# Kernel tuning notes

Hardware: AMD Instinct MI355X
Metric: run time of the kernel (lower is better)

## Reference

```python
import jax, jax.numpy as jnp
import numpy as np

B, CIN, T, H, W = 2, 256, 16, 16, 8
FF, COUT, NHEADS = 512, 256, 8
TEMP = 16.0
BN_EPS = 1e-5


def setup_inputs() -> dict:
    key = jax.random.key(0)
    ks = jax.random.split(key, 6)
    s_in = 1.0 / np.sqrt(CIN)
    s_ff = 1.0 / np.sqrt(FF)
    return {
        "x": jax.random.normal(ks[0], (B, CIN, T, H, W), jnp.float32),
        "WK": jax.random.uniform(ks[1], (FF, CIN), jnp.float32, -s_in, s_in),
        "WQ": jax.random.uniform(ks[2], (FF, CIN), jnp.float32, -s_in, s_in),
        "WV": jax.random.uniform(ks[3], (FF, CIN), jnp.float32, -s_in, s_in),
        "Wo": jax.random.uniform(ks[4], (COUT, FF), jnp.float32, -s_ff, s_ff),
        "bo": jax.random.uniform(ks[5], (COUT,), jnp.float32, -s_ff, s_ff),
        "gamma": jnp.ones((COUT,), jnp.float32),
        "beta": jnp.zeros((COUT,), jnp.float32),
    }


def reference(x, WK, WQ, WV, Wo, bo, gamma, beta):
    N = T * H * W
    xf = x.reshape(B, CIN, N)  # 1x1 conv3d == channel matmul
    dh = FF // NHEADS
    K = jnp.einsum("fc,bcn->bfn", WK, xf).reshape(B, NHEADS, dh, N)
    Q = jnp.einsum("fc,bcn->bfn", WQ, xf).reshape(B, NHEADS, dh, N)
    V = jnp.einsum("fc,bcn->bfn", WV, xf).reshape(B, NHEADS, dh, N)
    # KQ[b,h,i,j] = K_i . Q_j  (i = key token, j = query token, as in torch)
    KQ = jnp.einsum("bhdi,bhdj->bhij", K, Q) / TEMP
    # block-causal mask: token time index t = token_idx // (H*W); tril -> allow i >= j
    t_idx = jnp.arange(N) // (H * W)
    allow = t_idx[:, None] >= t_idx[None, :]  # (N, N)
    KQ = jnp.where(allow[None, None], KQ, -jnp.inf)
    attn = jax.nn.softmax(KQ, axis=3)  # softmax over j (last dim), as in torch
    # out[b,h,d,i] = sum_j V[b,h,d,j] * attn[b,h,i,j]
    Vo = jnp.einsum("bhdj,bhij->bhdi", V, attn).reshape(B, FF, N)
    y = jnp.einsum("of,bfn->bon", Wo, Vo) + bo[None, :, None]
    y = jax.nn.relu(y).reshape(B, COUT, T, H, W)
    out = x + y  # skip: out_dim == in_dim
    # BatchNorm3d (training-mode batch stats, biased var)
    mean = out.mean(axis=(0, 2, 3, 4), keepdims=True)
    var = out.var(axis=(0, 2, 3, 4), keepdims=True)
    norm = (out - mean) * jax.lax.rsqrt(var + BN_EPS)
    return norm * gamma[None, :, None, None, None] + beta[None, :, None, None, None]
```

## Files before the change

kernel.cpp:

```cpp
#include <hip/hip_runtime.h>
#include <math.h>

#define BB_   2
#define CIN_  256
#define NTOK_ 2048
#define FF_   512
#define COUT_ 256
#define NH_   8
#define DH_   64
#define HW_   128
#define BNEPS_ 1e-5f
#define SCALE_LOG2_ 0.09016844005556021f

typedef __attribute__((ext_vector_type(8))) short short8;
typedef __attribute__((ext_vector_type(4))) float f32x4;

__device__ inline unsigned short f2bf(float f) {
  union { float f; unsigned u; } v; v.f = f;
  unsigned r = (v.u + 0x7FFF + ((v.u >> 16) & 1)) >> 16;
  return (unsigned short)r;
}

__device__ __forceinline__ void dma16(const unsigned short* g, unsigned short* l) {
  __builtin_amdgcn_global_load_lds(
      (const __attribute__((address_space(1))) void*)g,
      (__attribute__((address_space(3))) void*)l, 16, 0, 0);
}

__global__ __launch_bounds__(256) void prep_kernel(
    const float* __restrict__ x, const float* __restrict__ WK,
    const float* __restrict__ WQ, const float* __restrict__ WV,
    const float* __restrict__ Wo, unsigned short* __restrict__ xT,
    unsigned short* __restrict__ Wkb, unsigned short* __restrict__ Wqb,
    unsigned short* __restrict__ Wvb, unsigned short* __restrict__ Wob) {
  __shared__ float T[64 * 65];
  const int tid = threadIdx.x;
  const int bid = blockIdx.x;
  if (bid < 256) {
    const int b = bid >> 7;
    const int rem = bid & 127;
    const int n0 = (rem >> 2) * 64;
    const int c0 = (rem & 3) * 64;
#pragma unroll
    for (int p = 0; p < 4; ++p) {
      const int idx = tid + 256 * p;
      const int row = idx >> 4, col = (idx & 15) * 4;
      const float4 v =
          *(const float4*)(x + (size_t)(b * CIN_ + c0 + row) * NTOK_ + n0 + col);
      T[row * 65 + col + 0] = v.x; T[row * 65 + col + 1] = v.y;
      T[row * 65 + col + 2] = v.z; T[row * 65 + col + 3] = v.w;
    }
    __syncthreads();
#pragma unroll
    for (int p = 0; p < 2; ++p) {
      const int idx = tid + 256 * p;
      const int nl = idx >> 3, c8 = (idx & 7) * 8;
      unsigned short u[8];
#pragma unroll
      for (int i = 0; i < 8; ++i) u[i] = f2bf(T[(c8 + i) * 65 + nl]);
      *(uint4*)(xT + ((size_t)(b * NTOK_ + n0 + nl)) * CIN_ + c0 + c8) =
          *(uint4*)u;
    }
  } else {
    const int t = bid - 256;
    const int which = t >> 5, blk = t & 31;
    const float* src = which == 0 ? WK : which == 1 ? WQ : which == 2 ? WV : Wo;
    unsigned short* dst = which == 0 ? Wkb : which == 1 ? Wqb : which == 2 ? Wvb : Wob;
    const int base = blk * 4096 + tid * 16;
#pragma unroll
    for (int p = 0; p < 4; ++p) {
      const float4 v = *(const float4*)(src + base + p * 4);
      ushort4 u;
      u.x = f2bf(v.x); u.y = f2bf(v.y); u.z = f2bf(v.z); u.w = f2bf(v.w);
      *(ushort4*)(dst + base + p * 4) = u;
    }
  }
}

__global__ __launch_bounds__(256, 2) void qkv_kernel(
    const unsigned short* __restrict__ xT, const unsigned short* __restrict__ Wkb,
    const unsigned short* __restrict__ Wqb, const unsigned short* __restrict__ Wvb,
    unsigned short* __restrict__ Kb, unsigned short* __restrict__ Qb,
    unsigned short* __restrict__ Vt) {
  __shared__ unsigned short Wsh[128 * 72];
  __shared__ unsigned short Xsh[128 * 72];
  const int tid = threadIdx.x;
  const int lane = tid & 63, w = tid >> 6;
  const int lx = lane & 15, q = lane >> 4;
  const int wm = w >> 1, wn = w & 1;
  const int n0 = blockIdx.x * 128;
  const int f0 = blockIdx.y * 128;
  const int b = blockIdx.z / 3, which = blockIdx.z % 3;
  const unsigned short* Wb = which == 0 ? Wkb : which == 1 ? Wqb : Wvb;

  const int srow = tid >> 3;
  const int soff = (tid & 7) * 8;
  const unsigned short* Wg = Wb + (size_t)(f0 + srow) * CIN_ + soff;
  const unsigned short* Xg = xT + ((size_t)(b * NTOK_ + n0 + srow)) * CIN_ + soff;

  uint4 wr[4], xr[4];
#pragma unroll
  for (int r = 0; r < 4; ++r) {
    wr[r] = *(const uint4*)(Wg + (size_t)(32 * r) * CIN_);
    xr[r] = *(const uint4*)(Xg + (size_t)(32 * r) * CIN_);
  }

  f32x4 acc[4][4];
#pragma unroll
  for (int i = 0; i < 4; ++i)
#pragma unroll
    for (int j = 0; j < 4; ++j) acc[i][j] = (f32x4){0.f, 0.f, 0.f, 0.f};

  for (int kk = 0; kk < 4; ++kk) {
    __syncthreads();
#pragma unroll
    for (int r = 0; r < 4; ++r) {
      *(uint4*)(Wsh + (srow + 32 * r) * 72 + soff) = wr[r];
      *(uint4*)(Xsh + (srow + 32 * r) * 72 + soff) = xr[r];
    }
    if (kk < 3) {
      const int c0 = (kk + 1) * 64;
#pragma unroll
      for (int r = 0; r < 4; ++r) {
        wr[r] = *(const uint4*)(Wg + (size_t)(32 * r) * CIN_ + c0);
        xr[r] = *(const uint4*)(Xg + (size_t)(32 * r) * CIN_ + c0);
      }
    }
    __syncthreads();
    short8 xF[4][2];
#pragma unroll
    for (int i = 0; i < 4; ++i) {
      xF[i][0] = *(const short8*)(Xsh + (64 * wn + 16 * i + lx) * 72 + q * 8);
      xF[i][1] = *(const short8*)(Xsh + (64 * wn + 16 * i + lx) * 72 + 32 + q * 8);
    }
    if (which < 2) {
#pragma unroll
      for (int i = 0; i < 4; ++i) {
        const short8 w0 = *(const short8*)(Wsh + (64 * wm + 16 * i + lx) * 72 + q * 8);
        const short8 w1 = *(const short8*)(Wsh + (64 * wm + 16 * i + lx) * 72 + 32 + q * 8);
#pragma unroll
        for (int j = 0; j < 4; ++j) {
          acc[i][j] = __builtin_amdgcn_mfma_f32_16x16x32_bf16(w0, xF[j][0], acc[i][j], 0, 0, 0);
          acc[i][j] = __builtin_amdgcn_mfma_f32_16x16x32_bf16(w1, xF[j][1], acc[i][j], 0, 0, 0);
        }
      }
    } else {
#pragma unroll
      for (int j = 0; j < 4; ++j) {
        const short8 w0 = *(const short8*)(Wsh + (64 * wm + 16 * j + lx) * 72 + q * 8);
        const short8 w1 = *(const short8*)(Wsh + (64 * wm + 16 * j + lx) * 72 + 32 + q * 8);
#pragma unroll
        for (int i = 0; i < 4; ++i) {
          acc[i][j] = __builtin_amdgcn_mfma_f32_16x16x32_bf16(xF[i][0], w0, acc[i][j], 0, 0, 0);
          acc[i][j] = __builtin_amdgcn_mfma_f32_16x16x32_bf16(xF[i][1], w1, acc[i][j], 0, 0, 0);
        }
      }
    }
  }

  const int h = (f0 >> 6) + wm;
  if (which < 2) {
    unsigned short* Y = (which == 0 ? Kb : Qb);
    const float sc = (which == 0) ? SCALE_LOG2_ : 1.0f;
#pragma unroll
    for (int i = 0; i < 4; ++i)
#pragma unroll
      for (int j = 0; j < 4; ++j) {
        const int n = n0 + 64 * wn + 16 * j + lx;
        const int d0 = 16 * i + 4 * q;
        ushort4 u;
        u.x = f2bf(acc[i][j][0] * sc); u.y = f2bf(acc[i][j][1] * sc);
        u.z = f2bf(acc[i][j][2] * sc); u.w = f2bf(acc[i][j][3] * sc);
        *(ushort4*)(Y + ((size_t)((b * NH_ + h) * NTOK_ + n)) * DH_ + d0) = u;
      }
  } else {
#pragma unroll
    for (int i = 0; i < 4; ++i)
#pragma unroll
      for (int j = 0; j < 4; ++j) {
        const int d = 16 * j + lx;
        const int n = n0 + 64 * wn + 16 * i + 4 * q;
        ushort4 u;
        u.x = f2bf(acc[i][j][0]); u.y = f2bf(acc[i][j][1]);
        u.z = f2bf(acc[i][j][2]); u.w = f2bf(acc[i][j][3]);
        *(ushort4*)(Vt + ((size_t)((b * NH_ + h) * DH_ + d)) * NTOK_ + n) = u;
      }
  }
}

__global__ __launch_bounds__(256, 3) void attn_kernel(
    const unsigned short* __restrict__ Kb, const unsigned short* __restrict__ Qb,
    const unsigned short* __restrict__ Vt, unsigned short* __restrict__ Ob) {
  __shared__ __align__(16) unsigned short Qbuf[2][4096];
  __shared__ __align__(16) unsigned short Vbuf[2][4096];
  __shared__ __align__(16) unsigned short Psh[4 * 16 * 72];

  const int tid = threadIdx.x;
  const int lane = tid & 63;
  const int w = tid >> 6;
  const int lx = lane & 15;
  const int q = lane >> 4;

  const int bid = blockIdx.x;
  const int u = bid >> 4;
  const int iblk = (u < 16) ? (31 - u) : (u - 16);
  const int bh = bid & 15;
  const int h = bh & 7, b = bh >> 3;
  const int i0 = iblk * 64;
  const int njt = ((iblk >> 1) + 1) * 2;

  const size_t bhs = (size_t)b * NH_ + h;
  const unsigned short* Kg = Kb + bhs * (size_t)NTOK_ * DH_ + (size_t)i0 * DH_;
  const unsigned short* Qg = Qb + bhs * (size_t)NTOK_ * DH_;
  const unsigned short* Vg = Vt + bhs * (size_t)DH_ * NTOK_;

  const int drow_lo = (lane >> 3);
  const int dcg = (lane & 7) ^ drow_lo;

  auto stage = [&](int buf, int j0) {
#pragma unroll
    for (int cc = 0; cc < 2; ++cc) {
      const int chunk = 2 * w + cc;
      const int row = chunk * 8 + drow_lo;
      dma16(Qg + (size_t)(j0 + row) * DH_ + dcg * 8, &Qbuf[buf][chunk * 512]);
      dma16(Vg + (size_t)row * NTOK_ + j0 + dcg * 8, &Vbuf[buf][chunk * 512]);
    }
  };

  const short8 aK0 = *(const short8*)(Kg + (16 * w + lx) * DH_ + q * 8);
  const short8 aK1 = *(const short8*)(Kg + (16 * w + lx) * DH_ + 32 + q * 8);

  unsigned short* Pw = Psh + w * 16 * 72;

  f32x4 o[4];
#pragma unroll
  for (int s = 0; s < 4; ++s) o[s] = (f32x4){0.f, 0.f, 0.f, 0.f};
  float rsum[4] = {0.f, 0.f, 0.f, 0.f};

  const int fr0 = ((q ^ (lx & 7)) << 3);
  const int fr1 = (((4 + q) ^ (lx & 7)) << 3);

  stage(0, 0);
  __syncthreads();

  int cur = 0;
  for (int jt = 0; jt < njt; ++jt) {
    if (jt + 1 < njt) stage(cur ^ 1, (jt + 1) * 64);

    const unsigned short* Qs = Qbuf[cur];
    const unsigned short* Vs = Vbuf[cur];

    f32x4 sa[4];
#pragma unroll
    for (int s = 0; s < 4; ++s) {
      const int row = 16 * s + lx;
      const short8 b0 = *(const short8*)(Qs + row * 64 + fr0);
      const short8 b1 = *(const short8*)(Qs + row * 64 + fr1);
      sa[s] = (f32x4){0.f, 0.f, 0.f, 0.f};
      sa[s] = __builtin_amdgcn_mfma_f32_16x16x32_bf16(aK0, b0, sa[s], 0, 0, 0);
      sa[s] = __builtin_amdgcn_mfma_f32_16x16x32_bf16(aK1, b1, sa[s], 0, 0, 0);
    }

#pragma unroll
    for (int s = 0; s < 4; ++s)
#pragma unroll
      for (int r = 0; r < 4; ++r) {
        const float p = __builtin_amdgcn_exp2f(sa[s][r]);
        rsum[r] += p;
        Pw[(q * 4 + r) * 72 + 16 * s + lx] =
            (unsigned short)(__builtin_bit_cast(unsigned, p) >> 16);
      }
    asm volatile("s_waitcnt lgkmcnt(0)" ::: "memory");

    const short8 pb0 = *(const short8*)(Pw + lx * 72 + q * 8);
    const short8 pb1 = *(const short8*)(Pw + lx * 72 + 32 + q * 8);
#pragma unroll
    for (int s = 0; s < 4; ++s) {
      const int row = 16 * s + lx;
      const short8 va0 = *(const short8*)(Vs + row * 64 + fr0);
      const short8 va1 = *(const short8*)(Vs + row * 64 + fr1);
      o[s] = __builtin_amdgcn_mfma_f32_16x16x32_bf16(va0, pb0, o[s], 0, 0, 0);
      o[s] = __builtin_amdgcn_mfma_f32_16x16x32_bf16(va1, pb1, o[s], 0, 0, 0);
    }

    __syncthreads();
    cur ^= 1;
  }

#pragma unroll
  for (int r = 0; r < 4; ++r) {
#pragma unroll
    for (int off = 1; off < 16; off <<= 1) rsum[r] += __shfl_xor(rsum[r], off);
  }
  const int gsrc = ((lx >> 2) << 4);
  const float u0 = __shfl(rsum[0], gsrc);
  const float u1 = __shfl(rsum[1], gsrc);
  const float u2 = __shfl(rsum[2], gsrc);
  const float u3 = __shfl(rsum[3], gsrc);
  const float lsel = (lx & 2) ? ((lx & 1) ? u3 : u2) : ((lx & 1) ? u1 : u0);
  const float invl = 1.0f / lsel;
  const int n = i0 + 16 * w + lx;
#pragma unroll
  for (int s = 0; s < 4; ++s) {
    ushort4 uo;
    uo.x = f2bf(o[s][0] * invl); uo.y = f2bf(o[s][1] * invl);
    uo.z = f2bf(o[s][2] * invl); uo.w = f2bf(o[s][3] * invl);
    *(ushort4*)(Ob + ((size_t)(b * NTOK_ + n)) * FF_ + h * 64 + 16 * s + 4 * q) = uo;
  }
}

__global__ __launch_bounds__(256) void proj_kernel(
    const unsigned short* __restrict__ Ob, const unsigned short* __restrict__ Wob,
    const float* __restrict__ bo, const float* __restrict__ x,
    float* __restrict__ pre) {
  __shared__ unsigned short Osh[64 * 72];
  __shared__ unsigned short Wsh[64 * 72];
  const int tid = threadIdx.x;
  const int lane = tid & 63, w = tid >> 6;
  const int lx = lane & 15, q = lane >> 4;
  const int wn = w & 1, wo = w >> 1;
  const int n0 = blockIdx.x * 64;
  const int o0 = blockIdx.y * 64;
  const int b = blockIdx.z;

  const int srow = tid >> 3;
  const int soff = (tid & 7) * 8;
  const unsigned short* Og = Ob + ((size_t)(b * NTOK_ + n0 + srow)) * FF_ + soff;
  const unsigned short* Wg = Wob + (size_t)(o0 + srow) * FF_ + soff;

  uint4 orr[2], wrr[2];
#pragma unroll
  for (int r = 0; r < 2; ++r) {
    orr[r] = *(const uint4*)(Og + (size_t)(32 * r) * FF_);
    wrr[r] = *(const uint4*)(Wg + (size_t)(32 * r) * FF_);
  }

  f32x4 acc[2][2];
#pragma unroll
  for (int i = 0; i < 2; ++i)
#pragma unroll
    for (int j = 0; j < 2; ++j) acc[i][j] = (f32x4){0.f, 0.f, 0.f, 0.f};

  for (int kk = 0; kk < 8; ++kk) {
    __syncthreads();
#pragma unroll
    for (int r = 0; r < 2; ++r) {
      *(uint4*)(Osh + (srow + 32 * r) * 72 + soff) = orr[r];
      *(uint4*)(Wsh + (srow + 32 * r) * 72 + soff) = wrr[r];
    }
    if (kk < 7) {
      const int c0 = (kk + 1) * 64;
#pragma unroll
      for (int r = 0; r < 2; ++r) {
        orr[r] = *(const uint4*)(Og + (size_t)(32 * r) * FF_ + c0);
        wrr[r] = *(const uint4*)(Wg + (size_t)(32 * r) * FF_ + c0);
      }
    }
    __syncthreads();
    short8 aF[2][2], bF[2][2];
#pragma unroll
    for (int i = 0; i < 2; ++i) {
      aF[i][0] = *(const short8*)(Osh + (32 * wn + 16 * i + lx) * 72 + q * 8);
      aF[i][1] = *(const short8*)(Osh + (32 * wn + 16 * i + lx) * 72 + 32 + q * 8);
      bF[i][0] = *(const short8*)(Wsh + (32 * wo + 16 * i + lx) * 72 + q * 8);
      bF[i][1] = *(const short8*)(Wsh + (32 * wo + 16 * i + lx) * 72 + 32 + q * 8);
    }
#pragma unroll
    for (int i = 0; i < 2; ++i)
#pragma unroll
      for (int j = 0; j < 2; ++j) {
        acc[i][j] = __builtin_amdgcn_mfma_f32_16x16x32_bf16(aF[i][0], bF[j][0], acc[i][j], 0, 0, 0);
        acc[i][j] = __builtin_amdgcn_mfma_f32_16x16x32_bf16(aF[i][1], bF[j][1], acc[i][j], 0, 0, 0);
      }
  }

#pragma unroll
  for (int j = 0; j < 2; ++j) {
    const int o = o0 + 32 * wo + 16 * j + lx;
    const float bias = bo[o];
#pragma unroll
    for (int i = 0; i < 2; ++i) {
      const int n = n0 + 32 * wn + 16 * i + 4 * q;
      const float4 xv = *(const float4*)(x + ((size_t)(b * CIN_ + o)) * NTOK_ + n);
      float4 v;
      v.x = fmaxf(acc[i][j][0] + bias, 0.f) + xv.x;
      v.y = fmaxf(acc[i][j][1] + bias, 0.f) + xv.y;
      v.z = fmaxf(acc[i][j][2] + bias, 0.f) + xv.z;
      v.w = fmaxf(acc[i][j][3] + bias, 0.f) + xv.w;
      *(float4*)(pre + ((size_t)(b * COUT_ + o)) * NTOK_ + n) = v;
    }
  }
}

__global__ __launch_bounds__(256) void bn_kernel(
    float* __restrict__ out, const float* __restrict__ gamma,
    const float* __restrict__ beta) {
  __shared__ float red[8];
  const int c = blockIdx.x;
  const int tid = threadIdx.x;
  const int lane = tid & 63, w = tid >> 6;

  float4 v[2][2];
  float s = 0.f, s2 = 0.f;
#pragma unroll
  for (int b = 0; b < BB_; ++b) {
    float* base = out + ((size_t)(b * COUT_ + c)) * NTOK_;
#pragma unroll
    for (int p = 0; p < 2; ++p) {
      const float4 t = *(const float4*)(base + 4 * tid + p * 1024);
      v[b][p] = t;
      s += t.x + t.y + t.z + t.w;
      s2 += t.x * t.x + t.y * t.y + t.z * t.z + t.w * t.w;
    }
  }
#pragma unroll
  for (int off = 32; off >= 1; off >>= 1) {
    s += __shfl_xor(s, off);
    s2 += __shfl_xor(s2, off);
  }
  if (lane == 0) { red[w] = s; red[4 + w] = s2; }
  __syncthreads();
  const float S = red[0] + red[1] + red[2] + red[3];
  const float S2 = red[4] + red[5] + red[6] + red[7];
  const float inv = 1.0f / (float)(BB_ * NTOK_);
  const float mean = S * inv;
  const float var = S2 * inv - mean * mean;
  const float sc = rsqrtf(var + BNEPS_) * gamma[c];
  const float bt = beta[c];
#pragma unroll
  for (int b = 0; b < BB_; ++b) {
    float* base = out + ((size_t)(b * COUT_ + c)) * NTOK_;
#pragma unroll
    for (int p = 0; p < 2; ++p) {
      float4 t = v[b][p];
      t.x = (t.x - mean) * sc + bt;
      t.y = (t.y - mean) * sc + bt;
      t.z = (t.z - mean) * sc + bt;
      t.w = (t.w - mean) * sc + bt;
      *(float4*)(base + 4 * tid + p * 1024) = t;
    }
  }
}

extern "C" void kernel_launch(void* const* d_in, const int* in_sizes, int n_in,
                              void* d_out, int out_size, void* d_ws, size_t ws_size,
                              hipStream_t stream) {
  (void)in_sizes; (void)n_in; (void)out_size; (void)ws_size;
  const float* x = (const float*)d_in[0];
  const float* WK = (const float*)d_in[1];
  const float* WQ = (const float*)d_in[2];
  const float* WV = (const float*)d_in[3];
  const float* Wo = (const float*)d_in[4];
  const float* bo = (const float*)d_in[5];
  const float* gamma = (const float*)d_in[6];
  const float* beta = (const float*)d_in[7];

  char* ws = (char*)d_ws;
  unsigned short* xT  = (unsigned short*)(ws);
  unsigned short* Wkb = (unsigned short*)(ws + 2097152);
  unsigned short* Wqb = (unsigned short*)(ws + 2359296);
  unsigned short* Wvb = (unsigned short*)(ws + 2621440);
  unsigned short* Wob = (unsigned short*)(ws + 2883584);
  unsigned short* Kb  = (unsigned short*)(ws + 3145728);
  unsigned short* Qb  = (unsigned short*)(ws + 7340032);
  unsigned short* Vt  = (unsigned short*)(ws + 11534336);
  unsigned short* Ob  = (unsigned short*)(ws + 15728640);
  float* out = (float*)d_out;

  prep_kernel<<<384, 256, 0, stream>>>(x, WK, WQ, WV, Wo, xT, Wkb, Wqb, Wvb, Wob);
  qkv_kernel<<<dim3(16, 4, 6), 256, 0, stream>>>(xT, Wkb, Wqb, Wvb, Kb, Qb, Vt);
  attn_kernel<<<dim3(512, 1, 1), 256, 0, stream>>>(Kb, Qb, Vt, Ob);
  proj_kernel<<<dim3(32, 4, 2), 256, 0, stream>>>(Ob, Wob, bo, x, out);
  bn_kernel<<<256, 256, 0, stream>>>(out, gamma, beta);
}
```

Measured before the change: 146.1 us.

## Halve QKV token tile for more blocks; widen attention key tiles to 128

The QKV projection kernel now uses 64-token tiles instead of 128, which doubles the grid to 768 blocks, and raises its occupancy target to 3. The attention kernel now stages 128-column Q/V tiles per iteration with a re-derived XOR swizzle, which halves the number of loop iterations and barriers, and processes the P·V step in two halves that reuse the per-wave P buffer. The larger attention LDS footprint lowers its occupancy target from 3 to 2 blocks per CU, and the bigger tiles add more work per step on the causal diagonal.

```diff
diff --git a/kernel.cpp b/kernel.cpp
--- a/kernel.cpp
+++ b/kernel.cpp
@@ -77,18 +77,18 @@
   }
 }
 
-__global__ __launch_bounds__(256, 2) void qkv_kernel(
+__global__ __launch_bounds__(256, 3) void qkv_kernel(
     const unsigned short* __restrict__ xT, const unsigned short* __restrict__ Wkb,
     const unsigned short* __restrict__ Wqb, const unsigned short* __restrict__ Wvb,
     unsigned short* __restrict__ Kb, unsigned short* __restrict__ Qb,
     unsigned short* __restrict__ Vt) {
   __shared__ unsigned short Wsh[128 * 72];
-  __shared__ unsigned short Xsh[128 * 72];
+  __shared__ unsigned short Xsh[64 * 72];
   const int tid = threadIdx.x;
   const int lane = tid & 63, w = tid >> 6;
   const int lx = lane & 15, q = lane >> 4;
   const int wm = w >> 1, wn = w & 1;
-  const int n0 = blockIdx.x * 128;
+  const int n0 = blockIdx.x * 64;
   const int f0 = blockIdx.y * 128;
   const int b = blockIdx.z / 3, which = blockIdx.z % 3;
   const unsigned short* Wb = which == 0 ? Wkb : which == 1 ? Wqb : Wvb;
@@ -98,40 +98,37 @@
   const unsigned short* Wg = Wb + (size_t)(f0 + srow) * CIN_ + soff;
   const unsigned short* Xg = xT + ((size_t)(b * NTOK_ + n0 + srow)) * CIN_ + soff;
 
-  uint4 wr[4], xr[4];
-#pragma unroll
-  for (int r = 0; r < 4; ++r) {
-    wr[r] = *(const uint4*)(Wg + (size_t)(32 * r) * CIN_);
-    xr[r] = *(const uint4*)(Xg + (size_t)(32 * r) * CIN_);
-  }
-
-  f32x4 acc[4][4];
+  uint4 wr[4], xr[2];
+#pragma unroll
+  for (int r = 0; r < 4; ++r) wr[r] = *(const uint4*)(Wg + (size_t)(32 * r) * CIN_);
+#pragma unroll
+  for (int r = 0; r < 2; ++r) xr[r] = *(const uint4*)(Xg + (size_t)(32 * r) * CIN_);
+
+  f32x4 acc[4][2];
 #pragma unroll
   for (int i = 0; i < 4; ++i)
 #pragma unroll
-    for (int j = 0; j < 4; ++j) acc[i][j] = (f32x4){0.f, 0.f, 0.f, 0.f};
+    for (int j = 0; j < 2; ++j) acc[i][j] = (f32x4){0.f, 0.f, 0.f, 0.f};
 
   for (int kk = 0; kk < 4; ++kk) {
     __syncthreads();
 #pragma unroll
-    for (int r = 0; r < 4; ++r) {
-      *(uint4*)(Wsh + (srow + 32 * r) * 72 + soff) = wr[r];
-      *(uint4*)(Xsh + (srow + 32 * r) * 72 + soff) = xr[r];
-    }
+    for (int r = 0; r < 4; ++r) *(uint4*)(Wsh + (srow + 32 * r) * 72 + soff) = wr[r];
+#pragma unroll
+    for (int r = 0; r < 2; ++r) *(uint4*)(Xsh + (srow + 32 * r) * 72 + soff) = xr[r];
     if (kk < 3) {
       const int c0 = (kk + 1) * 64;
 #pragma unroll
-      for (int r = 0; r < 4; ++r) {
-        wr[r] = *(const uint4*)(Wg + (size_t)(32 * r) * CIN_ + c0);
-        xr[r] = *(const uint4*)(Xg + (size_t)(32 * r) * CIN_ + c0);
-      }
-    }
-    __syncthreads();
-    short8 xF[4][2];
-#pragma unroll
-    for (int i = 0; i < 4; ++i) {
-      xF[i][0] = *(const short8*)(Xsh + (64 * wn + 16 * i + lx) * 72 + q * 8);
-      xF[i][1] = *(const short8*)(Xsh + (64 * wn + 16 * i + lx) * 72 + 32 + q * 8);
+      for (int r = 0; r < 4; ++r) wr[r] = *(const uint4*)(Wg + (size_t)(32 * r) * CIN_ + c0);
+#pragma unroll
+      for (int r = 0; r < 2; ++r) xr[r] = *(const uint4*)(Xg + (size_t)(32 * r) * CIN_ + c0);
+    }
+    __syncthreads();
+    short8 xF[2][2];
+#pragma unroll
+    for (int i = 0; i < 2; ++i) {
+      xF[i][0] = *(const short8*)(Xsh + (32 * wn + 16 * i + lx) * 72 + q * 8);
+      xF[i][1] = *(const short8*)(Xsh + (32 * wn + 16 * i + lx) * 72 + 32 + q * 8);
     }
     if (which < 2) {
 #pragma unroll
@@ -139,20 +136,20 @@
         const short8 w0 = *(const short8*)(Wsh + (64 * wm + 16 * i + lx) * 72 + q * 8);
         const short8 w1 = *(const short8*)(Wsh + (64 * wm + 16 * i + lx) * 72 + 32 + q * 8);
 #pragma unroll
-        for (int j = 0; j < 4; ++j) {
+        for (int j = 0; j < 2; ++j) {
           acc[i][j] = __builtin_amdgcn_mfma_f32_16x16x32_bf16(w0, xF[j][0], acc[i][j], 0, 0, 0);
           acc[i][j] = __builtin_amdgcn_mfma_f32_16x16x32_bf16(w1, xF[j][1], acc[i][j], 0, 0, 0);
         }
       }
     } else {
 #pragma unroll
-      for (int j = 0; j < 4; ++j) {
-        const short8 w0 = *(const short8*)(Wsh + (64 * wm + 16 * j + lx) * 72 + q * 8);
-        const short8 w1 = *(const short8*)(Wsh + (64 * wm + 16 * j + lx) * 72 + 32 + q * 8);
-#pragma unroll
-        for (int i = 0; i < 4; ++i) {
-          acc[i][j] = __builtin_amdgcn_mfma_f32_16x16x32_bf16(xF[i][0], w0, acc[i][j], 0, 0, 0);
-          acc[i][j] = __builtin_amdgcn_mfma_f32_16x16x32_bf16(xF[i][1], w1, acc[i][j], 0, 0, 0);
+      for (int jf = 0; jf < 4; ++jf) {
+        const short8 w0 = *(const short8*)(Wsh + (64 * wm + 16 * jf + lx) * 72 + q * 8);
+        const short8 w1 = *(const short8*)(Wsh + (64 * wm + 16 * jf + lx) * 72 + 32 + q * 8);
+#pragma unroll
+        for (int i = 0; i < 2; ++i) {
+          acc[jf][i] = __builtin_amdgcn_mfma_f32_16x16x32_bf16(xF[i][0], w0, acc[jf][i], 0, 0, 0);
+          acc[jf][i] = __builtin_amdgcn_mfma_f32_16x16x32_bf16(xF[i][1], w1, acc[jf][i], 0, 0, 0);
         }
       }
     }
@@ -165,8 +162,8 @@
 #pragma unroll
     for (int i = 0; i < 4; ++i)
 #pragma unroll
-      for (int j = 0; j < 4; ++j) {
-        const int n = n0 + 64 * wn + 16 * j + lx;
+      for (int j = 0; j < 2; ++j) {
+        const int n = n0 + 32 * wn + 16 * j + lx;
         const int d0 = 16 * i + 4 * q;
         ushort4 u;
         u.x = f2bf(acc[i][j][0] * sc); u.y = f2bf(acc[i][j][1] * sc);
@@ -175,24 +172,24 @@
       }
   } else {
 #pragma unroll
-    for (int i = 0; i < 4; ++i)
-#pragma unroll
-      for (int j = 0; j < 4; ++j) {
-        const int d = 16 * j + lx;
-        const int n = n0 + 64 * wn + 16 * i + 4 * q;
+    for (int jf = 0; jf < 4; ++jf)
+#pragma unroll
+      for (int i = 0; i < 2; ++i) {
+        const int d = 16 * jf + lx;
+        const int n = n0 + 32 * wn + 16 * i + 4 * q;
         ushort4 u;
-        u.x = f2bf(acc[i][j][0]); u.y = f2bf(acc[i][j][1]);
-        u.z = f2bf(acc[i][j][2]); u.w = f2bf(acc[i][j][3]);
+        u.x = f2bf(acc[jf][i][0]); u.y = f2bf(acc[jf][i][1]);
+        u.z = f2bf(acc[jf][i][2]); u.w = f2bf(acc[jf][i][3]);
         *(ushort4*)(Vt + ((size_t)((b * NH_ + h) * DH_ + d)) * NTOK_ + n) = u;
       }
   }
 }
 
-__global__ __launch_bounds__(256, 3) void attn_kernel(
+__global__ __launch_bounds__(256, 2) void attn_kernel(
     const unsigned short* __restrict__ Kb, const unsigned short* __restrict__ Qb,
     const unsigned short* __restrict__ Vt, unsigned short* __restrict__ Ob) {
-  __shared__ __align__(16) unsigned short Qbuf[2][4096];
-  __shared__ __align__(16) unsigned short Vbuf[2][4096];
+  __shared__ __align__(16) unsigned short Qbuf[2][8192];
+  __shared__ __align__(16) unsigned short Vbuf[2][8192];
   __shared__ __align__(16) unsigned short Psh[4 * 16 * 72];
 
   const int tid = threadIdx.x;
@@ -207,23 +204,27 @@
   const int bh = bid & 15;
   const int h = bh & 7, b = bh >> 3;
   const int i0 = iblk * 64;
-  const int njt = ((iblk >> 1) + 1) * 2;
+  const int njt = (iblk >> 1) + 1;
 
   const size_t bhs = (size_t)b * NH_ + h;
   const unsigned short* Kg = Kb + bhs * (size_t)NTOK_ * DH_ + (size_t)i0 * DH_;
   const unsigned short* Qg = Qb + bhs * (size_t)NTOK_ * DH_;
   const unsigned short* Vg = Vt + bhs * (size_t)DH_ * NTOK_;
 
-  const int drow_lo = (lane >> 3);
-  const int dcg = (lane & 7) ^ drow_lo;
-
   auto stage = [&](int buf, int j0) {
 #pragma unroll
-    for (int cc = 0; cc < 2; ++cc) {
-      const int chunk = 2 * w + cc;
-      const int row = chunk * 8 + drow_lo;
-      dma16(Qg + (size_t)(j0 + row) * DH_ + dcg * 8, &Qbuf[buf][chunk * 512]);
-      dma16(Vg + (size_t)row * NTOK_ + j0 + dcg * 8, &Vbuf[buf][chunk * 512]);
+    for (int cc = 0; cc < 4; ++cc) {
+      const int chunk = 4 * w + cc;
+      {
+        const int row = chunk * 8 + (lane >> 3);
+        const int grp = (lane & 7) ^ (row & 7);
+        dma16(Qg + (size_t)(j0 + row) * DH_ + grp * 8, &Qbuf[buf][chunk * 512]);
+      }
+      {
+        const int row = chunk * 4 + (lane >> 4);
+        const int grp = (lane & 15) ^ (row & 7);
+        dma16(Vg + (size_t)row * NTOK_ + j0 + grp * 8, &Vbuf[buf][chunk * 512]);
+      }
     }
   };
 
@@ -239,20 +240,23 @@
 
   const int fr0 = ((q ^ (lx & 7)) << 3);
   const int fr1 = (((4 + q) ^ (lx & 7)) << 3);
+  int frv[4];
+#pragma unroll
+  for (int kk = 0; kk < 4; ++kk) frv[kk] = (((4 * kk + q) ^ (lx & 7)) << 3);
 
   stage(0, 0);
   __syncthreads();
 
   int cur = 0;
   for (int jt = 0; jt < njt; ++jt) {
-    if (jt + 1 < njt) stage(cur ^ 1, (jt + 1) * 64);
+    if (jt + 1 < njt) stage(cur ^ 1, (jt + 1) * 128);
 
     const unsigned short* Qs = Qbuf[cur];
     const unsigned short* Vs = Vbuf[cur];
 
-    f32x4 sa[4];
-#pragma unroll
-    for (int s = 0; s < 4; ++s) {
+    f32x4 sa[8];
+#pragma unroll
+    for (int s = 0; s < 8; ++s) {
       const int row = 16 * s + lx;
       const short8 b0 = *(const short8*)(Qs + row * 64 + fr0);
       const short8 b1 = *(const short8*)(Qs + row * 64 + fr1);
@@ -262,25 +266,29 @@
     }
 
 #pragma unroll
-    for (int s = 0; s < 4; ++s)
-#pragma unroll
-      for (int r = 0; r < 4; ++r) {
-        const float p = __builtin_amdgcn_exp2f(sa[s][r]);
-        rsum[r] += p;
-        Pw[(q * 4 + r) * 72 + 16 * s + lx] =
-            (unsigned short)(__builtin_bit_cast(unsigned, p) >> 16);
-      }
-    asm volatile("s_waitcnt lgkmcnt(0)" ::: "memory");
-
-    const short8 pb0 = *(const short8*)(Pw + lx * 72 + q * 8);
-    const short8 pb1 = *(const short8*)(Pw + lx * 72 + 32 + q * 8);
-#pragma unroll
-    for (int s = 0; s < 4; ++s) {
-      const int row = 16 * s + lx;
-      const short8 va0 = *(const short8*)(Vs + row * 64 + fr0);
-      const short8 va1 = *(const short8*)(Vs + row * 64 + fr1);
-      o[s] = __builtin_amdgcn_mfma_f32_16x16x32_bf16(va0, pb0, o[s], 0, 0, 0);
-      o[s] = __builtin_amdgcn_mfma_f32_16x16x32_bf16(va1, pb1, o[s], 0, 0, 0);
+    for (int half = 0; half < 2; ++half) {
+#pragma unroll
+      for (int s2 = 0; s2 < 4; ++s2)
+#pragma unroll
+        for (int r = 0; r < 4; ++r) {
+          const float p = __builtin_amdgcn_exp2f(sa[4 * half + s2][r]);
+          rsum[r] += p;
+          Pw[(q * 4 + r) * 72 + 16 * s2 + lx] =
+              (unsigned short)(__builtin_bit_cast(unsigned, p) >> 16);
+        }
+      asm volatile("s_waitcnt lgkmcnt(0)" ::: "memory");
+
+      const short8 pb0 = *(const short8*)(Pw + lx * 72 + q * 8);
+      const short8 pb1 = *(const short8*)(Pw + lx * 72 + 32 + q * 8);
+#pragma unroll
+      for (int s = 0; s < 4; ++s) {
+        const int row = 16 * s + lx;
+        const short8 va0 = *(const short8*)(Vs + row * 128 + frv[2 * half + 0]);
+        const short8 va1 = *(const short8*)(Vs + row * 128 + frv[2 * half + 1]);
+        o[s] = __builtin_amdgcn_mfma_f32_16x16x32_bf16(va0, pb0, o[s], 0, 0, 0);
+        o[s] = __builtin_amdgcn_mfma_f32_16x16x32_bf16(va1, pb1, o[s], 0, 0, 0);
+      }
+      asm volatile("" ::: "memory");
     }
 
     __syncthreads();
@@ -468,7 +476,7 @@
   float* out = (float*)d_out;
 
   prep_kernel<<<384, 256, 0, stream>>>(x, WK, WQ, WV, Wo, xT, Wkb, Wqb, Wvb, Wob);
-  qkv_kernel<<<dim3(16, 4, 6), 256, 0, stream>>>(xT, Wkb, Wqb, Wvb, Kb, Qb, Vt);
+  qkv_kernel<<<dim3(32, 4, 6), 256, 0, stream>>>(xT, Wkb, Wqb, Wvb, Kb, Qb, Vt);
   attn_kernel<<<dim3(512, 1, 1), 256, 0, stream>>>(Kb, Qb, Vt, Ob);
   proj_kernel<<<dim3(32, 4, 2), 256, 0, stream>>>(Ob, Wob, bo, x, out);
   bn_kernel<<<256, 256, 0, stream>>>(out, gamma, beta);
```

Result: faster. 142.0 us (-2.8%).
